# Optimization experiments

Hardware: AMD Instinct MI355X
Metric: run time of the kernel (lower is better)

## Reference

```python
import jax, jax.numpy as jnp
import numpy as np

N_USERS = 100000
N_LOCAS = 50000
N = N_USERS + N_LOCAS
D = 128   # embedding_dynamic_size
K = 128   # kg entity dim
S = 128   # static dim
NK = 50000  # kg rows
E = 2048  # number of events
LN_EPS = 1e-5
NORM_EPS = 1e-12


def setup_inputs() -> dict:
    key = jax.random.key(0)
    ks = jax.random.split(key, 24)
    f = jnp.float32
    rin = D + K + 1
    s_rnn = 1.0 / np.sqrt(D)
    s_pred = 1.0 / np.sqrt(2 * S + 2 * D + K)
    inp = {
        'embedding': jax.random.normal(ks[0], (N, D), f),
        'static': jax.random.normal(ks[1], (N, S), f),
        'kg': jax.random.normal(ks[2], (NK, K), f),
        'W_ih_u': jax.random.normal(ks[3], (D, rin), f) * s_rnn,
        'b_ih_u': jax.random.normal(ks[4], (D,), f) * s_rnn,
        'W_hh_u': jax.random.normal(ks[5], (D, D), f) * s_rnn,
        'b_hh_u': jax.random.normal(ks[6], (D,), f) * s_rnn,
        'W_ih_l': jax.random.normal(ks[7], (D, rin), f) * s_rnn,
        'b_ih_l': jax.random.normal(ks[8], (D,), f) * s_rnn,
        'W_hh_l': jax.random.normal(ks[9], (D, D), f) * s_rnn,
        'b_hh_l': jax.random.normal(ks[10], (D,), f) * s_rnn,
        'w_proj': jax.random.normal(ks[11], (D,), f),   # NormalLinear(1, D) weight, std=1/sqrt(1)=1
        'b_proj': jax.random.normal(ks[12], (D,), f),
        'ln_g': jnp.ones((D + K,), f),
        'ln_b': jnp.zeros((D + K,), f),
        'W_pred': jax.random.normal(ks[13], (S + D, 2 * S + 2 * D + K), f) * s_pred,
        'b_pred': jnp.zeros((S + D,), f),
        'delta_u': jax.random.uniform(ks[14], (E,), f),
        'delta_l': jax.random.uniform(ks[15], (E,), f),
        'idx_user': jax.random.randint(ks[16], (E,), 0, N_USERS, jnp.int32),
        'idx_loca': jax.random.randint(ks[17], (E,), 0, N_LOCAS, jnp.int32),
        'idx_prev': jax.random.randint(ks[18], (E,), 0, N_LOCAS, jnp.int32),
        'idx_know': jax.random.randint(ks[19], (E,), 0, NK, jnp.int32),
        'num_users': N_USERS,
    }
    return inp


def reference(embedding, static, kg, W_ih_u, b_ih_u, W_hh_u, b_hh_u,
              W_ih_l, b_ih_l, W_hh_l, b_hh_l, w_proj, b_proj, ln_g, ln_b,
              W_pred, b_pred, delta_u, delta_l,
              idx_user, idx_loca, idx_prev, idx_know, num_users):
    sg = jax.lax.stop_gradient

    def l2n(x):  # F.normalize along the feature dim (row vector)
        return x / jnp.maximum(jnp.linalg.norm(x), NORM_EPS)

    # event index preprocessing (matches idx_loca + num_users etc.)
    xs = (idx_user, idx_loca + num_users, idx_prev + num_users, idx_know,
          delta_u, delta_l)

    def step(carry, ev):
        emb, loss = carry
        iu, il, ip, ik, du, dl = ev
        u = emb[iu]        # [D]
        l = emb[il]        # [D]
        p = emb[ip]        # [D]
        kgr = kg[ik]       # [K]
        # projection: u * (1 + Linear(1->D)(delta_u))
        proj = u * (1.0 + w_proj * du + b_proj)
        # layer_norm over concat([emb_prev, kg_row]) of size D+K
        x = jnp.concatenate([p, kgr])
        mu = x.mean()
        var = jnp.mean((x - mu) ** 2)
        ln = (x - mu) / jnp.sqrt(var + LN_EPS) * ln_g + ln_b
        meta = jnp.concatenate([proj, ln, static[ip], static[iu]])  # [2S+2D+K]
        pred = W_pred @ meta + b_pred                               # [S+D]
        tgt = jnp.concatenate([l, static[il]])
        loss_pred = jnp.mean((pred - sg(tgt)) ** 2)
        # RNNCell updates (tanh), then L2-normalize
        x_u = jnp.concatenate([l, kgr, du[None]])
        new_u = l2n(jnp.tanh(W_ih_u @ x_u + b_ih_u + W_hh_u @ u + b_hh_u))
        x_l = jnp.concatenate([u, kgr, dl[None]])
        new_l = l2n(jnp.tanh(W_ih_l @ x_l + b_ih_l + W_hh_l @ l + b_hh_l))
        loss = loss + loss_pred \
                    + jnp.mean((new_u - sg(u)) ** 2) \
                    + jnp.mean((new_l - sg(l)) ** 2)
        emb = emb.at[iu].set(new_u).at[il].set(new_l)
        return (emb, loss), None

    (emb, loss), _ = jax.lax.scan(
        step, (embedding, jnp.asarray(0.0, embedding.dtype)), xs)
    return emb, loss
```

## Files before the change

kernel.cpp:

```cpp
#include <hip/hip_runtime.h>

#define DEVINL static __device__ __forceinline__

typedef float f32x4 __attribute__((ext_vector_type(4)));

constexpr int NUSER = 100000;
constexpr int D     = 128;
constexpr int METAN = 640;
constexpr int NT    = 256;
constexpr int CH    = 4;
constexpr int KP4   = 160;
constexpr int KR4   = 96;
constexpr int NCPY  = 2048;
constexpr int STW   = 640;

struct Params {
  const float *emb_in, *stat, *kg;
  const float *Wihu, *bihu, *Whhu, *bhhu;
  const float *Wihl, *bihl, *Whhl, *bhhl;
  const float *wproj, *bproj, *lng, *lnb, *Wpred, *bpred;
  const float *deltau, *deltal;
  const int *idxu, *idxl, *idxp, *idxk;
  float *emb;
  float *loss_slot;
  float *WpredT;
  float *WrnnT;
  float *brnn;
  float *wcol;
  float *loss_ev;
  float *stash;
  int *cnt_u, *cnt_w, *cnt_t;
  int *flag_u, *flag_l;
  int E, N, NLOC, NWORK;
};

DEVINL float loadx(const float* p) {
  return __hip_atomic_load(p, __ATOMIC_RELAXED, __HIP_MEMORY_SCOPE_AGENT);
}
DEVINL void storex(float* p, float v) {
  __hip_atomic_store(p, v, __ATOMIC_RELAXED, __HIP_MEMORY_SCOPE_AGENT);
}
DEVINL int loadcnt(const int* p) {
  return __hip_atomic_load(p, __ATOMIC_RELAXED, __HIP_MEMORY_SCOPE_AGENT);
}
DEVINL void sigadd(int* pp) {
  __hip_atomic_fetch_add(pp, 1, __ATOMIC_RELAXED, __HIP_MEMORY_SCOPE_AGENT);
}
DEVINL float dot4(float4 a, float4 b) { return a.x*b.x + a.y*b.y + a.z*b.z + a.w*b.w; }

DEVINL float4 block_sum4(float4 v, float4* s4) {
  #pragma unroll
  for (int o = 32; o; o >>= 1) {
    v.x += __shfl_xor(v.x, o, 64); v.y += __shfl_xor(v.y, o, 64);
    v.z += __shfl_xor(v.z, o, 64); v.w += __shfl_xor(v.w, o, 64);
  }
  if ((threadIdx.x & 63) == 0) s4[threadIdx.x >> 6] = v;
  __syncthreads();
  float4 r;
  r.x = s4[0].x + s4[1].x + s4[2].x + s4[3].x;
  r.y = s4[0].y + s4[1].y + s4[2].y + s4[3].y;
  r.z = s4[0].z + s4[1].z + s4[2].z + s4[3].z;
  r.w = s4[0].w + s4[1].w + s4[2].w + s4[3].w;
  __syncthreads();
  return r;
}

DEVINL void half_sum4(float4 v, float4* s4, float4* lo, float4* hi) {
  #pragma unroll
  for (int o = 32; o; o >>= 1) {
    v.x += __shfl_xor(v.x, o, 64); v.y += __shfl_xor(v.y, o, 64);
    v.z += __shfl_xor(v.z, o, 64); v.w += __shfl_xor(v.w, o, 64);
  }
  if ((threadIdx.x & 63) == 0) s4[threadIdx.x >> 6] = v;
  __syncthreads();
  lo->x = s4[0].x + s4[1].x; lo->y = s4[0].y + s4[1].y;
  lo->z = s4[0].z + s4[1].z; lo->w = s4[0].w + s4[1].w;
  hi->x = s4[2].x + s4[3].x; hi->y = s4[2].y + s4[3].y;
  hi->z = s4[2].z + s4[3].z; hi->w = s4[2].w + s4[3].w;
  __syncthreads();
}

__global__ void k_init(Params p) {
  int tid = blockIdx.x * NT + threadIdx.x;
  int stride = gridDim.x * NT;
  for (int e = tid; e < p.E; e += stride) {
    p.flag_u[p.idxu[e]] = 1;
    p.flag_l[p.idxl[e]] = 1;
  }
  for (int idx = tid; idx < 256 * KP4; idx += stride) {
    int j = idx / KP4, k4 = idx - j * KP4;
    float4 v = *(const float4*)(p.Wpred + (size_t)j * METAN + k4 * 4);
    ((float4*)p.WpredT)[k4 * 256 + j] = v;
  }
  for (int idx = tid; idx < 256 * KR4; idx += stride) {
    int j = idx / KR4, k4 = idx - j * KR4;
    int i = j & 127;
    const float* Wih = (j < 128) ? p.Wihu : p.Wihl;
    const float* Whh = (j < 128) ? p.Whhu : p.Whhl;
    float4 v; float* vp = (float*)&v;
    #pragma unroll
    for (int e = 0; e < 4; ++e) {
      int k = k4 * 4 + e;
      vp[e] = (k < 256) ? Wih[(size_t)i * 257 + k] : Whh[(size_t)i * 128 + (k - 256)];
    }
    ((float4*)p.WrnnT)[k4 * 256 + j] = v;
  }
  for (int j = tid; j < 256; j += stride) {
    int i = j & 127;
    p.brnn[j] = (j < 128) ? p.bihu[i] + p.bhhu[i] : p.bihl[i] + p.bhhl[i];
    p.wcol[j] = (j < 128) ? p.Wihu[(size_t)i * 257 + 256] : p.Wihl[(size_t)i * 257 + 256];
  }
}

__global__ __launch_bounds__(NT) void k_copy(Params p) {
  size_t gid = (size_t)blockIdx.x * NT + threadIdx.x;
  size_t gs  = (size_t)gridDim.x * NT;
  size_t n4  = (size_t)p.N * 32;
  const f32x4* src = (const f32x4*)p.emb_in;
  f32x4* dst = (f32x4*)p.emb;
  size_t g = gid;
  for (; g + 3 * gs < n4; g += 4 * gs) {
    size_t g0 = g, g1 = g + gs, g2 = g + 2 * gs, g3 = g + 3 * gs;
    int r0 = (int)(g0 >> 5), r1 = (int)(g1 >> 5), r2 = (int)(g2 >> 5), r3 = (int)(g3 >> 5);
    int f0 = (r0 < NUSER) ? p.flag_u[r0] : p.flag_l[r0 - NUSER];
    int f1 = (r1 < NUSER) ? p.flag_u[r1] : p.flag_l[r1 - NUSER];
    int f2 = (r2 < NUSER) ? p.flag_u[r2] : p.flag_l[r2 - NUSER];
    int f3 = (r3 < NUSER) ? p.flag_u[r3] : p.flag_l[r3 - NUSER];
    f32x4 v0 = src[g0], v1 = src[g1], v2 = src[g2], v3 = src[g3];
    if (!f0) dst[g0] = v0;
    if (!f1) dst[g1] = v1;
    if (!f2) dst[g2] = v2;
    if (!f3) dst[g3] = v3;
  }
  for (; g < n4; g += gs) {
    int r = (int)(g >> 5);
    int f = (r < NUSER) ? p.flag_u[r] : p.flag_l[r - NUSER];
    f32x4 v = src[g];
    if (!f) dst[g] = v;
  }
}

__global__ __launch_bounds__(NT, 2) void k_chain(Params p) {
  __shared__ __align__(16) float s_u[CH][D], s_l[CH][D], s_p[CH][D], s_kg[CH][D];
  __shared__ float4 s_r4[4];
  __shared__ unsigned long long s_redu[4][CH];
  __shared__ int s_ev[8][CH];
  __shared__ float s_dd[2][CH];

  const int tid = threadIdx.x, w = tid >> 6, lane = tid & 63;
  const int c = blockIdx.x;
  const int base = c * CH;
  const int nev = min(CH, p.E - base);
  if (nev <= 0) return;

  int iu_[CH], il_[CH], ip_[CH], ik_[CH];
  float du_[CH], dl_[CH];
  #pragma unroll
  for (int e = 0; e < CH; ++e) {
    int t = base + e; bool v = e < nev;
    iu_[e] = v ? p.idxu[t] : -1;
    il_[e] = v ? p.idxl[t] : -1;
    ip_[e] = v ? p.idxp[t] : -1;
    ik_[e] = v ? p.idxk[t] : 0;
    du_[e] = v ? p.deltau[t] : 0.f;
    dl_[e] = v ? p.deltal[t] : 0.f;
  }

  unsigned long long pk[CH] = {0ull,0ull,0ull,0ull};
  for (int s = tid; s < base; s += NT) {
    int ius = p.idxu[s], ils = p.idxl[s], ips = p.idxp[s];
    #pragma unroll
    for (int e = 0; e < CH; ++e) {
      unsigned long long a  = (ius == iu_[e]);
      unsigned long long wl = (ils == il_[e]);
      unsigned long long b  = (unsigned long long)((ils == il_[e]) + (ips == il_[e]));
      unsigned long long cc = (ils == ip_[e]);
      pk[e] += a | (wl << 16) | (b << 32) | (cc << 48);
    }
  }
  #pragma unroll
  for (int o = 32; o; o >>= 1) {
    #pragma unroll
    for (int e = 0; e < CH; ++e) pk[e] += __shfl_xor(pk[e], o, 64);
  }
  if (lane == 0) {
    #pragma unroll
    for (int e = 0; e < CH; ++e) s_redu[w][e] = pk[e];
  }
  __syncthreads();
  #pragma unroll
  for (int e = 0; e < CH; ++e)
    pk[e] = s_redu[0][e] + s_redu[1][e] + s_redu[2][e] + s_redu[3][e];
  __syncthreads();

  int A_[CH], WL_[CH], B_[CH], C_[CH];
  #pragma unroll
  for (int e = 0; e < CH; ++e) {
    int a  = (int)(pk[e] & 0xffff),        wl = (int)((pk[e] >> 16) & 0xffff);
    int b  = (int)((pk[e] >> 32) & 0xffff), cc = (int)((pk[e] >> 48) & 0xffff);
    #pragma unroll
    for (int s2 = 0; s2 < CH; ++s2) if (s2 < e) {
      a  += (iu_[s2] == iu_[e]);
      wl += (il_[s2] == il_[e]);
      b  += (il_[s2] == il_[e]) + (ip_[s2] == il_[e]);
      cc += (il_[s2] == ip_[e]);
    }
    A_[e] = a; WL_[e] = wl; B_[e] = b; C_[e] = cc;
  }
  bool internal = false;
  #pragma unroll
  for (int t2 = 1; t2 < CH; ++t2) if (t2 < nev) {
    #pragma unroll
    for (int s2 = 0; s2 < t2; ++s2)
      internal |= (iu_[s2] == iu_[t2]) | (il_[s2] == il_[t2]) |
                  (il_[s2] == ip_[t2]) | (ip_[s2] == il_[t2]);
  }

  if (tid == 0) {
    #pragma unroll
    for (int e = 0; e < CH; ++e) {
      s_ev[0][e] = iu_[e]; s_ev[1][e] = il_[e]; s_ev[2][e] = ip_[e];
      s_ev[3][e] = A_[e];  s_ev[4][e] = WL_[e]; s_ev[5][e] = B_[e];
      s_ev[6][e] = C_[e];  s_ev[7][e] = ik_[e];
      s_dd[0][e] = du_[e]; s_dd[1][e] = dl_[e];
    }
  }
  __syncthreads();

  auto PRELOAD = [&](int b0, int b1) {
    int e = w;
    if (e >= b0 && e < b1) {
      int iu = s_ev[0][e], ilr = s_ev[1][e] + NUSER, ipr = s_ev[2][e] + NUSER;
      int A = s_ev[3][e], WL = s_ev[4][e], Ck = s_ev[6][e], ik = s_ev[7][e];
      if (lane < 32) {
        int li = lane * 4;
        *(float4*)&s_kg[e][li] = *(const float4*)(p.kg + (size_t)ik * D + li);
      }
      int i0 = lane * 2;
      if (!A)  *(float2*)&s_u[e][i0] = *(const float2*)(p.emb_in + (size_t)iu  * D + i0);
      if (!WL) *(float2*)&s_l[e][i0] = *(const float2*)(p.emb_in + (size_t)ilr * D + i0);
      if (!Ck) *(float2*)&s_p[e][i0] = *(const float2*)(p.emb_in + (size_t)ipr * D + i0);
    }
  };

  auto SPIN = [&](int b0, int b1) {
    if (w == 0) {
      int e = b0 + lane;
      bool act = lane < (b1 - b0);
      int iu = 0, il = 0, ip = 0, A = 0, Bc = 0, Cc = 0;
      if (act) {
        iu = s_ev[0][e]; il = s_ev[1][e]; ip = s_ev[2][e];
        A = s_ev[3][e]; Bc = s_ev[5][e]; Cc = s_ev[6][e];
      }
      int guard = 0;
      while (true) {
        int x = loadcnt(&p.cnt_u[iu]);
        int y = loadcnt(&p.cnt_t[il]);
        int z = loadcnt(&p.cnt_w[ip]);
        bool ok = (!act) | ((x >= A) & (y >= Bc) & (z >= Cc));
        if (__all(ok)) break;
        if (++guard > (1 << 22)) break;
        __builtin_amdgcn_s_sleep(1);
      }
    }
    __syncthreads();
  };

  auto POSTLOAD = [&](int b0, int b1) {
    int e = w;
    if (e >= b0 && e < b1) {
      int iu = s_ev[0][e], ilr = s_ev[1][e] + NUSER, ipr = s_ev[2][e] + NUSER;
      int A = s_ev[3][e], WL = s_ev[4][e], Ck = s_ev[6][e];
      int i0 = lane * 2;
      if (A) {
        s_u[e][i0]   = loadx(p.emb + (size_t)iu * D + i0);
        s_u[e][i0+1] = loadx(p.emb + (size_t)iu * D + i0 + 1);
      }
      if (WL) {
        s_l[e][i0]   = loadx(p.emb + (size_t)ilr * D + i0);
        s_l[e][i0+1] = loadx(p.emb + (size_t)ilr * D + i0 + 1);
      }
      if (Ck) {
        s_p[e][i0]   = loadx(p.emb + (size_t)ipr * D + i0);
        s_p[e][i0+1] = loadx(p.emb + (size_t)ipr * D + i0 + 1);
      }
    }
  };

  auto RNNPROC = [&](int b0, int b1) {
    __syncthreads();
    const bool uc = (tid < 128);
    const float4* xo0 = (const float4*)(uc ? s_l[0] : s_u[0]);
    const float4* xo1 = (const float4*)(uc ? s_l[1] : s_u[1]);
    const float4* xo2 = (const float4*)(uc ? s_l[2] : s_u[2]);
    const float4* xo3 = (const float4*)(uc ? s_l[3] : s_u[3]);
    const float4* xk0 = (const float4*)s_kg[0];
    const float4* xk1 = (const float4*)s_kg[1];
    const float4* xk2 = (const float4*)s_kg[2];
    const float4* xk3 = (const float4*)s_kg[3];
    const float4* xs0 = (const float4*)(uc ? s_u[0] : s_l[0]);
    const float4* xs1 = (const float4*)(uc ? s_u[1] : s_l[1]);
    const float4* xs2 = (const float4*)(uc ? s_u[2] : s_l[2]);
    const float4* xs3 = (const float4*)(uc ? s_u[3] : s_l[3]);
    float ra0 = 0.f, ra1 = 0.f, ra2 = 0.f, ra3 = 0.f;
    const float4* wr = (const float4*)p.WrnnT + tid;
    #pragma unroll 8
    for (int k4 = 0; k4 < 32; ++k4) {
      float4 wv = wr[k4 * 256];
      ra0 += dot4(wv, xo0[k4]); ra1 += dot4(wv, xo1[k4]);
      ra2 += dot4(wv, xo2[k4]); ra3 += dot4(wv, xo3[k4]);
    }
    #pragma unroll 8
    for (int k4 = 32; k4 < 64; ++k4) {
      float4 wv = wr[k4 * 256];
      ra0 += dot4(wv, xk0[k4-32]); ra1 += dot4(wv, xk1[k4-32]);
      ra2 += dot4(wv, xk2[k4-32]); ra3 += dot4(wv, xk3[k4-32]);
    }
    #pragma unroll 8
    for (int k4 = 64; k4 < 96; ++k4) {
      float4 wv = wr[k4 * 256];
      ra0 += dot4(wv, xs0[k4-64]); ra1 += dot4(wv, xs1[k4-64]);
      ra2 += dot4(wv, xs2[k4-64]); ra3 += dot4(wv, xs3[k4-64]);
    }
    float brn = p.brnn[tid], wcv = p.wcol[tid];
    float d0 = uc ? s_dd[0][0] : s_dd[1][0];
    float d1 = uc ? s_dd[0][1] : s_dd[1][1];
    float d2 = uc ? s_dd[0][2] : s_dd[1][2];
    float d3 = uc ? s_dd[0][3] : s_dd[1][3];
    float h0 = tanhf(ra0 + brn + wcv * d0), h1 = tanhf(ra1 + brn + wcv * d1);
    float h2v = tanhf(ra2 + brn + wcv * d2), h3 = tanhf(ra3 + brn + wcv * d3);

    float4 SU, SL;
    half_sum4(make_float4(h0*h0, h1*h1, h2v*h2v, h3*h3), s_r4, &SU, &SL);
    float s0 = uc ? SU.x : SL.x, s1 = uc ? SU.y : SL.y;
    float s2 = uc ? SU.z : SL.z, s3 = uc ? SU.w : SL.w;
    float n0 = h0 / fmaxf(sqrtf(s0), 1e-12f), n1 = h1 / fmaxf(sqrtf(s1), 1e-12f);
    float n2 = h2v / fmaxf(sqrtf(s2), 1e-12f), n3 = h3 / fmaxf(sqrtf(s3), 1e-12f);

    float nv[CH] = {n0, n1, n2, n3};
    #pragma unroll
    for (int e = 0; e < CH; ++e) if (e >= b0 && e < b1) {
      if (tid < 128) storex(p.emb + (size_t)s_ev[0][e] * D + tid, nv[e]);
      else           storex(p.emb + ((size_t)s_ev[1][e] + NUSER) * D + (tid - 128), nv[e]);
    }
    __syncthreads();

    if (tid >= b0 && tid < b1) {
      __builtin_amdgcn_fence(__ATOMIC_RELEASE, "agent");
      sigadd(&p.cnt_u[s_ev[0][tid]]);
      sigadd(&p.cnt_t[s_ev[1][tid]]);
      sigadd(&p.cnt_w[s_ev[1][tid]]);
      sigadd(&p.cnt_t[s_ev[2][tid]]);
    }

    #pragma unroll
    for (int e = 0; e < CH; ++e) if (e >= b0 && e < b1) {
      float* st = p.stash + (size_t)(base + e) * STW;
      if (tid < 128) {
        st[tid]       = s_u[e][tid];
        st[256 + tid] = s_p[e][tid];
        st[384 + tid] = nv[e];
      } else {
        int i = tid - 128;
        st[128 + i] = s_l[e][i];
        st[512 + i] = nv[e];
      }
    }
  };

  if (!internal) {
    PRELOAD(0, nev);
    SPIN(0, nev);
    POSTLOAD(0, nev);
    RNNPROC(0, nev);
  } else {
    for (int e = 0; e < nev; ++e) {
      PRELOAD(e, e + 1);
      SPIN(e, e + 1);
      POSTLOAD(e, e + 1);
      RNNPROC(e, e + 1);
    }
  }
}

__global__ __launch_bounds__(NT, 2) void k_loss(Params p) {
  __shared__ __align__(16) float s_meta[CH][METAN];
  __shared__ __align__(16) float s_u[CH][D], s_l[CH][D], s_p[CH][D], s_kg[CH][D], s_sil[CH][D];
  __shared__ float4 s_r4[4];

  const int tid = threadIdx.x, w = tid >> 6, lane = tid & 63;
  const int c = blockIdx.x;
  const int base = c * CH;
  const int nev = min(CH, p.E - base);
  if (nev <= 0) return;

  if (w < nev) {
    int e = w;
    int t = base + e;
    int iu = p.idxu[t], ilr = p.idxl[t] + NUSER, ipr = p.idxp[t] + NUSER, ik = p.idxk[t];
    const float* st = p.stash + (size_t)t * STW;
    int i0 = lane * 2;
    *(float2*)&s_u[e][i0] = *(const float2*)(st + i0);
    *(float2*)&s_l[e][i0] = *(const float2*)(st + 128 + i0);
    *(float2*)&s_p[e][i0] = *(const float2*)(st + 256 + i0);
    int h2 = lane >> 5, li = (lane & 31) * 4;
    if (h2 == 0) {
      *(float4*)&s_kg[e][li]         = *(const float4*)(p.kg   + (size_t)ik  * D + li);
      *(float4*)&s_meta[e][512 + li] = *(const float4*)(p.stat + (size_t)iu  * D + li);
    } else {
      *(float4*)&s_meta[e][384 + li] = *(const float4*)(p.stat + (size_t)ipr * D + li);
      *(float4*)&s_sil[e][li]        = *(const float4*)(p.stat + (size_t)ilr * D + li);
    }
  }
  __syncthreads();

  if (w < nev) {
    int e = w;
    float du = p.deltau[base + e];
    float4 xv = (lane < 32) ? *(const float4*)&s_p[e][lane * 4]
                            : *(const float4*)&s_kg[e][(lane - 32) * 4];
    float sm = xv.x + xv.y + xv.z + xv.w;
    #pragma unroll
    for (int o = 32; o; o >>= 1) sm += __shfl_xor(sm, o, 64);
    float mu = sm * (1.f / 256.f);
    float4 d = make_float4(xv.x - mu, xv.y - mu, xv.z - mu, xv.w - mu);
    float vs = d.x*d.x + d.y*d.y + d.z*d.z + d.w*d.w;
    #pragma unroll
    for (int o = 32; o; o >>= 1) vs += __shfl_xor(vs, o, 64);
    float rstd = rsqrtf(vs * (1.f / 256.f) + 1e-5f);
    int idx2 = lane * 4;
    float4 g  = *(const float4*)&p.lng[idx2];
    float4 bb = *(const float4*)&p.lnb[idx2];
    *(float4*)&s_meta[e][128 + idx2] = make_float4(
      d.x*rstd*g.x + bb.x, d.y*rstd*g.y + bb.y,
      d.z*rstd*g.z + bb.z, d.w*rstd*g.w + bb.w);
    int i0 = lane * 2;
    #pragma unroll
    for (int j = 0; j < 2; ++j) {
      int i = i0 + j;
      s_meta[e][i] = s_u[e][i] * (1.f + p.wproj[i] * du + p.bproj[i]);
    }
  }
  __syncthreads();

  const bool uc = (tid < 128);
  const float4* m40 = (const float4*)&s_meta[0][0];
  const float4* m41 = (const float4*)&s_meta[1][0];
  const float4* m42 = (const float4*)&s_meta[2][0];
  const float4* m43 = (const float4*)&s_meta[3][0];
  float pa0 = 0.f, pa1 = 0.f, pa2 = 0.f, pa3 = 0.f;
  const float4* wp = (const float4*)p.WpredT + tid;
  #pragma unroll 8
  for (int k4 = 0; k4 < KP4; ++k4) {
    float4 wv = wp[k4 * 256];
    pa0 += dot4(wv, m40[k4]); pa1 += dot4(wv, m41[k4]);
    pa2 += dot4(wv, m42[k4]); pa3 += dot4(wv, m43[k4]);
  }
  float bp = p.bpred[tid];
  float4 ep2;
  {
    float tg0 = uc ? s_l[0][tid] : s_sil[0][tid - 128];
    float tg1 = uc ? s_l[1][tid] : s_sil[1][tid - 128];
    float tg2 = uc ? s_l[2][tid] : s_sil[2][tid - 128];
    float tg3 = uc ? s_l[3][tid] : s_sil[3][tid - 128];
    float e0 = pa0 + bp - tg0, e1 = pa1 + bp - tg1;
    float e2 = pa2 + bp - tg2, e3 = pa3 + bp - tg3;
    ep2 = make_float4(e0*e0, e1*e1, e2*e2, e3*e3);
  }
  float4 LP = block_sum4(ep2, s_r4);

  const float* st0 = p.stash + (size_t)(base + 0) * STW;
  const float* st1 = p.stash + (size_t)(base + 1) * STW;
  const float* st2 = p.stash + (size_t)(base + 2) * STW;
  const float* st3 = p.stash + (size_t)(base + 3) * STW;
  int noff = uc ? (384 + tid) : (512 + tid - 128);
  float n0 = st0[noff], n1 = (nev > 1) ? st1[noff] : 0.f;
  float n2 = (nev > 2) ? st2[noff] : 0.f, n3 = (nev > 3) ? st3[noff] : 0.f;
  float o0 = uc ? s_u[0][tid] : s_l[0][tid - 128];
  float o1 = uc ? s_u[1][tid] : s_l[1][tid - 128];
  float o2 = uc ? s_u[2][tid] : s_l[2][tid - 128];
  float o3 = uc ? s_u[3][tid] : s_l[3][tid - 128];
  float q0 = n0 - o0, q1 = n1 - o1, q2 = n2 - o2, q3 = n3 - o3;
  float4 LE = block_sum4(make_float4(q0*q0, q1*q1, q2*q2, q3*q3), s_r4);

  if (tid < nev) {
    float lp = (tid == 0) ? LP.x : (tid == 1) ? LP.y : (tid == 2) ? LP.z : LP.w;
    float le = (tid == 0) ? LE.x : (tid == 1) ? LE.y : (tid == 2) ? LE.z : LE.w;
    p.loss_ev[base + tid] = lp * (1.f / 256.f) + le * (1.f / 128.f);
  }
}

__global__ void k_fin(Params p) {
  __shared__ float4 s_r4[4];
  float v = 0.f;
  for (int i = threadIdx.x; i < p.E; i += NT) v += p.loss_ev[i];
  float4 r = block_sum4(make_float4(v, 0.f, 0.f, 0.f), s_r4);
  if (threadIdx.x == 0) p.loss_slot[0] = r.x;
}

extern "C" void kernel_launch(void* const* d_in, const int* in_sizes, int n_in,
                              void* d_out, int out_size, void* d_ws, size_t ws_size,
                              hipStream_t stream) {
  Params p;
  p.emb_in = (const float*)d_in[0];
  p.stat   = (const float*)d_in[1];
  p.kg     = (const float*)d_in[2];
  p.Wihu = (const float*)d_in[3];   p.bihu = (const float*)d_in[4];
  p.Whhu = (const float*)d_in[5];   p.bhhu = (const float*)d_in[6];
  p.Wihl = (const float*)d_in[7];   p.bihl = (const float*)d_in[8];
  p.Whhl = (const float*)d_in[9];   p.bhhl = (const float*)d_in[10];
  p.wproj = (const float*)d_in[11]; p.bproj = (const float*)d_in[12];
  p.lng  = (const float*)d_in[13];  p.lnb  = (const float*)d_in[14];
  p.Wpred = (const float*)d_in[15]; p.bpred = (const float*)d_in[16];
  p.deltau = (const float*)d_in[17];
  p.deltal = (const float*)d_in[18];
  p.idxu = (const int*)d_in[19];
  p.idxl = (const int*)d_in[20];
  p.idxp = (const int*)d_in[21];
  p.idxk = (const int*)d_in[22];

  p.E    = in_sizes[17];
  p.N    = in_sizes[0] / D;
  p.NLOC = p.N - NUSER;
  p.NWORK = (p.E + CH - 1) / CH;

  p.emb       = (float*)d_out;
  p.loss_slot = (float*)d_out + (size_t)p.N * D;

  char* ws = (char*)d_ws;
  size_t off = 0;
  auto take = [&](size_t bytes) {
    void* r = ws + off;
    off += (bytes + 255) & ~(size_t)255;
    return r;
  };
  p.WpredT  = (float*)take((size_t)KP4 * 256 * 16);
  p.WrnnT   = (float*)take((size_t)KR4 * 256 * 16);
  p.brnn    = (float*)take(256 * 4);
  p.wcol    = (float*)take(256 * 4);
  p.loss_ev = (float*)take((size_t)p.E * 4);
  p.stash   = (float*)take((size_t)p.E * STW * 4);
  size_t z0 = off;
  p.cnt_u   = (int*)take((size_t)NUSER * 4);
  p.cnt_w   = (int*)take((size_t)p.NLOC * 4);
  p.cnt_t   = (int*)take((size_t)p.NLOC * 4);
  p.flag_u  = (int*)take((size_t)NUSER * 4);
  p.flag_l  = (int*)take((size_t)p.NLOC * 4);
  size_t zbytes = off - z0;

  hipMemsetAsync(ws + z0, 0, zbytes, stream);
  hipLaunchKernelGGL(k_init,  dim3(512),     dim3(NT), 0, stream, p);
  hipLaunchKernelGGL(k_chain, dim3(p.NWORK), dim3(NT), 0, stream, p);
  hipLaunchKernelGGL(k_copy,  dim3(NCPY),    dim3(NT), 0, stream, p);
  hipLaunchKernelGGL(k_loss,  dim3(p.NWORK), dim3(NT), 0, stream, p);
  hipLaunchKernelGGL(k_fin,   dim3(1),       dim3(NT), 0, stream, p);
}
```

Before: 178.2 us.

## Split chain into scan, dependency-free easy pass, and spinning hard pass

Measured after the change: 150.3 us. -15.6%, faster.

```diff
diff --git a/kernel.cpp b/kernel.cpp
--- a/kernel.cpp
+++ b/kernel.cpp
@@ -13,6 +13,7 @@
 constexpr int KR4   = 96;
 constexpr int NCPY  = 2048;
 constexpr int STW   = 640;
+constexpr int CIW   = 20;
 
 struct Params {
   const float *emb_in, *stat, *kg;
@@ -29,6 +30,7 @@
   float *wcol;
   float *loss_ev;
   float *stash;
+  int *cinfo;
   int *cnt_u, *cnt_w, *cnt_t;
   int *flag_u, *flag_l;
   int E, N, NLOC, NWORK;
@@ -112,60 +114,21 @@
   }
 }
 
-__global__ __launch_bounds__(NT) void k_copy(Params p) {
-  size_t gid = (size_t)blockIdx.x * NT + threadIdx.x;
-  size_t gs  = (size_t)gridDim.x * NT;
-  size_t n4  = (size_t)p.N * 32;
-  const f32x4* src = (const f32x4*)p.emb_in;
-  f32x4* dst = (f32x4*)p.emb;
-  size_t g = gid;
-  for (; g + 3 * gs < n4; g += 4 * gs) {
-    size_t g0 = g, g1 = g + gs, g2 = g + 2 * gs, g3 = g + 3 * gs;
-    int r0 = (int)(g0 >> 5), r1 = (int)(g1 >> 5), r2 = (int)(g2 >> 5), r3 = (int)(g3 >> 5);
-    int f0 = (r0 < NUSER) ? p.flag_u[r0] : p.flag_l[r0 - NUSER];
-    int f1 = (r1 < NUSER) ? p.flag_u[r1] : p.flag_l[r1 - NUSER];
-    int f2 = (r2 < NUSER) ? p.flag_u[r2] : p.flag_l[r2 - NUSER];
-    int f3 = (r3 < NUSER) ? p.flag_u[r3] : p.flag_l[r3 - NUSER];
-    f32x4 v0 = src[g0], v1 = src[g1], v2 = src[g2], v3 = src[g3];
-    if (!f0) dst[g0] = v0;
-    if (!f1) dst[g1] = v1;
-    if (!f2) dst[g2] = v2;
-    if (!f3) dst[g3] = v3;
-  }
-  for (; g < n4; g += gs) {
-    int r = (int)(g >> 5);
-    int f = (r < NUSER) ? p.flag_u[r] : p.flag_l[r - NUSER];
-    f32x4 v = src[g];
-    if (!f) dst[g] = v;
-  }
-}
-
-__global__ __launch_bounds__(NT, 2) void k_chain(Params p) {
-  __shared__ __align__(16) float s_u[CH][D], s_l[CH][D], s_p[CH][D], s_kg[CH][D];
-  __shared__ float4 s_r4[4];
+__global__ __launch_bounds__(NT) void k_scan(Params p) {
   __shared__ unsigned long long s_redu[4][CH];
-  __shared__ int s_ev[8][CH];
-  __shared__ float s_dd[2][CH];
-
   const int tid = threadIdx.x, w = tid >> 6, lane = tid & 63;
-  const int c = blockIdx.x;
-  const int base = c * CH;
+  const int c = blockIdx.x, base = c * CH;
   const int nev = min(CH, p.E - base);
   if (nev <= 0) return;
 
-  int iu_[CH], il_[CH], ip_[CH], ik_[CH];
-  float du_[CH], dl_[CH];
+  int iu_[CH], il_[CH], ip_[CH];
   #pragma unroll
   for (int e = 0; e < CH; ++e) {
     int t = base + e; bool v = e < nev;
     iu_[e] = v ? p.idxu[t] : -1;
     il_[e] = v ? p.idxl[t] : -1;
     ip_[e] = v ? p.idxp[t] : -1;
-    ik_[e] = v ? p.idxk[t] : 0;
-    du_[e] = v ? p.deltau[t] : 0.f;
-    dl_[e] = v ? p.deltal[t] : 0.f;
-  }
-
+  }
   unsigned long long pk[CH] = {0ull,0ull,0ull,0ull};
   for (int s = tid; s < base; s += NT) {
     int ius = p.idxu[s], ils = p.idxl[s], ips = p.idxp[s];
@@ -191,38 +154,178 @@
   #pragma unroll
   for (int e = 0; e < CH; ++e)
     pk[e] = s_redu[0][e] + s_redu[1][e] + s_redu[2][e] + s_redu[3][e];
-  __syncthreads();
-
-  int A_[CH], WL_[CH], B_[CH], C_[CH];
+
+  if (tid == 0) {
+    int* ci = p.cinfo + (size_t)c * CIW;
+    bool internal = false;
+    #pragma unroll
+    for (int t2 = 1; t2 < CH; ++t2) if (t2 < nev) {
+      #pragma unroll
+      for (int s2 = 0; s2 < t2; ++s2)
+        internal |= (iu_[s2] == iu_[t2]) | (il_[s2] == il_[t2]) |
+                    (il_[s2] == ip_[t2]) | (ip_[s2] == il_[t2]);
+    }
+    bool clean = !internal;
+    #pragma unroll
+    for (int e = 0; e < CH; ++e) {
+      int a  = (int)(pk[e] & 0xffff),        wl = (int)((pk[e] >> 16) & 0xffff);
+      int b  = (int)((pk[e] >> 32) & 0xffff), cc = (int)((pk[e] >> 48) & 0xffff);
+      #pragma unroll
+      for (int s2 = 0; s2 < CH; ++s2) if (s2 < e) {
+        a  += (iu_[s2] == iu_[e]);
+        wl += (il_[s2] == il_[e]);
+        b  += (il_[s2] == il_[e]) + (ip_[s2] == il_[e]);
+        cc += (il_[s2] == ip_[e]);
+      }
+      ci[e] = a; ci[4 + e] = wl; ci[8 + e] = b; ci[12 + e] = cc;
+      if (e < nev) clean = clean && (a == 0) && (b == 0) && (cc == 0);
+    }
+    ci[16] = internal ? 1 : 0;
+    ci[17] = clean ? 1 : 0;
+  }
+}
+
+__global__ __launch_bounds__(NT, 2) void k_easy(Params p) {
+  __shared__ __align__(16) float s_u[CH][D], s_l[CH][D], s_p[CH][D], s_kg[CH][D];
+  __shared__ float4 s_r4[4];
+  __shared__ int s_ev[3][CH];
+  __shared__ float s_dd[2][CH];
+
+  const int tid = threadIdx.x, w = tid >> 6, lane = tid & 63;
+  const int c = blockIdx.x, base = c * CH;
+  const int nev = min(CH, p.E - base);
+  if (nev <= 0) return;
+  if (!p.cinfo[(size_t)c * CIW + 17]) return;
+
+  if (tid == 0) {
+    #pragma unroll
+    for (int e = 0; e < CH; ++e) {
+      int t = base + e; bool v = e < nev;
+      s_ev[0][e] = v ? p.idxu[t] : 0;
+      s_ev[1][e] = v ? p.idxl[t] : 0;
+      s_ev[2][e] = v ? p.idxk[t] : 0;
+      s_dd[0][e] = v ? p.deltau[t] : 0.f;
+      s_dd[1][e] = v ? p.deltal[t] : 0.f;
+    }
+  }
+  __syncthreads();
+
+  if (w < nev) {
+    int e = w;
+    int t = base + e;
+    int iu = s_ev[0][e], ilr = s_ev[1][e] + NUSER, ipr = p.idxp[t] + NUSER, ik = s_ev[2][e];
+    if (lane < 32) {
+      int li = lane * 4;
+      *(float4*)&s_kg[e][li] = *(const float4*)(p.kg + (size_t)ik * D + li);
+    }
+    int i0 = lane * 2;
+    *(float2*)&s_u[e][i0] = *(const float2*)(p.emb_in + (size_t)iu  * D + i0);
+    *(float2*)&s_l[e][i0] = *(const float2*)(p.emb_in + (size_t)ilr * D + i0);
+    *(float2*)&s_p[e][i0] = *(const float2*)(p.emb_in + (size_t)ipr * D + i0);
+  }
+  __syncthreads();
+
+  const bool uc = (tid < 128);
+  const float4* xo0 = (const float4*)(uc ? s_l[0] : s_u[0]);
+  const float4* xo1 = (const float4*)(uc ? s_l[1] : s_u[1]);
+  const float4* xo2 = (const float4*)(uc ? s_l[2] : s_u[2]);
+  const float4* xo3 = (const float4*)(uc ? s_l[3] : s_u[3]);
+  const float4* xk0 = (const float4*)s_kg[0];
+  const float4* xk1 = (const float4*)s_kg[1];
+  const float4* xk2 = (const float4*)s_kg[2];
+  const float4* xk3 = (const float4*)s_kg[3];
+  const float4* xs0 = (const float4*)(uc ? s_u[0] : s_l[0]);
+  const float4* xs1 = (const float4*)(uc ? s_u[1] : s_l[1]);
+  const float4* xs2 = (const float4*)(uc ? s_u[2] : s_l[2]);
+  const float4* xs3 = (const float4*)(uc ? s_u[3] : s_l[3]);
+  float ra0 = 0.f, ra1 = 0.f, ra2 = 0.f, ra3 = 0.f;
+  const float4* wr = (const float4*)p.WrnnT + tid;
+  #pragma unroll 8
+  for (int k4 = 0; k4 < 32; ++k4) {
+    float4 wv = wr[k4 * 256];
+    ra0 += dot4(wv, xo0[k4]); ra1 += dot4(wv, xo1[k4]);
+    ra2 += dot4(wv, xo2[k4]); ra3 += dot4(wv, xo3[k4]);
+  }
+  #pragma unroll 8
+  for (int k4 = 32; k4 < 64; ++k4) {
+    float4 wv = wr[k4 * 256];
+    ra0 += dot4(wv, xk0[k4-32]); ra1 += dot4(wv, xk1[k4-32]);
+    ra2 += dot4(wv, xk2[k4-32]); ra3 += dot4(wv, xk3[k4-32]);
+  }
+  #pragma unroll 8
+  for (int k4 = 64; k4 < 96; ++k4) {
+    float4 wv = wr[k4 * 256];
+    ra0 += dot4(wv, xs0[k4-64]); ra1 += dot4(wv, xs1[k4-64]);
+    ra2 += dot4(wv, xs2[k4-64]); ra3 += dot4(wv, xs3[k4-64]);
+  }
+  float brn = p.brnn[tid], wcv = p.wcol[tid];
+  float d0 = uc ? s_dd[0][0] : s_dd[1][0];
+  float d1 = uc ? s_dd[0][1] : s_dd[1][1];
+  float d2 = uc ? s_dd[0][2] : s_dd[1][2];
+  float d3 = uc ? s_dd[0][3] : s_dd[1][3];
+  float h0 = tanhf(ra0 + brn + wcv * d0), h1 = tanhf(ra1 + brn + wcv * d1);
+  float h2v = tanhf(ra2 + brn + wcv * d2), h3 = tanhf(ra3 + brn + wcv * d3);
+
+  float4 SU, SL;
+  half_sum4(make_float4(h0*h0, h1*h1, h2v*h2v, h3*h3), s_r4, &SU, &SL);
+  float s0 = uc ? SU.x : SL.x, s1 = uc ? SU.y : SL.y;
+  float s2 = uc ? SU.z : SL.z, s3 = uc ? SU.w : SL.w;
+  float n0 = h0 / fmaxf(sqrtf(s0), 1e-12f), n1 = h1 / fmaxf(sqrtf(s1), 1e-12f);
+  float n2 = h2v / fmaxf(sqrtf(s2), 1e-12f), n3 = h3 / fmaxf(sqrtf(s3), 1e-12f);
+
+  float nv[CH] = {n0, n1, n2, n3};
   #pragma unroll
-  for (int e = 0; e < CH; ++e) {
-    int a  = (int)(pk[e] & 0xffff),        wl = (int)((pk[e] >> 16) & 0xffff);
-    int b  = (int)((pk[e] >> 32) & 0xffff), cc = (int)((pk[e] >> 48) & 0xffff);
-    #pragma unroll
-    for (int s2 = 0; s2 < CH; ++s2) if (s2 < e) {
-      a  += (iu_[s2] == iu_[e]);
-      wl += (il_[s2] == il_[e]);
-      b  += (il_[s2] == il_[e]) + (ip_[s2] == il_[e]);
-      cc += (il_[s2] == ip_[e]);
-    }
-    A_[e] = a; WL_[e] = wl; B_[e] = b; C_[e] = cc;
-  }
-  bool internal = false;
-  #pragma unroll
-  for (int t2 = 1; t2 < CH; ++t2) if (t2 < nev) {
-    #pragma unroll
-    for (int s2 = 0; s2 < t2; ++s2)
-      internal |= (iu_[s2] == iu_[t2]) | (il_[s2] == il_[t2]) |
-                  (il_[s2] == ip_[t2]) | (ip_[s2] == il_[t2]);
-  }
+  for (int e = 0; e < CH; ++e) if (e < nev) {
+    if (tid < 128) p.emb[(size_t)s_ev[0][e] * D + tid] = nv[e];
+    else           p.emb[((size_t)s_ev[1][e] + NUSER) * D + (tid - 128)] = nv[e];
+    float* st = p.stash + (size_t)(base + e) * STW;
+    if (tid < 128) {
+      st[tid]       = s_u[e][tid];
+      st[256 + tid] = s_p[e][tid];
+      st[384 + tid] = nv[e];
+    } else {
+      int i = tid - 128;
+      st[128 + i] = s_l[e][i];
+      st[512 + i] = nv[e];
+    }
+  }
+
+  if (tid < nev) {
+    sigadd(&p.cnt_u[s_ev[0][tid]]);
+    sigadd(&p.cnt_t[s_ev[1][tid]]);
+    sigadd(&p.cnt_w[s_ev[1][tid]]);
+    sigadd(&p.cnt_t[p.idxp[base + tid]]);
+  }
+}
+
+__global__ __launch_bounds__(NT, 2) void k_hard(Params p) {
+  __shared__ __align__(16) float s_u[CH][D], s_l[CH][D], s_p[CH][D], s_kg[CH][D];
+  __shared__ float4 s_r4[4];
+  __shared__ int s_ev[8][CH];
+  __shared__ float s_dd[2][CH];
+
+  const int tid = threadIdx.x, w = tid >> 6, lane = tid & 63;
+  const int c = blockIdx.x, base = c * CH;
+  const int nev = min(CH, p.E - base);
+  if (nev <= 0) return;
+  const int* ci = p.cinfo + (size_t)c * CIW;
+  if (ci[17]) return;
+  const bool internal = ci[16];
 
   if (tid == 0) {
     #pragma unroll
     for (int e = 0; e < CH; ++e) {
-      s_ev[0][e] = iu_[e]; s_ev[1][e] = il_[e]; s_ev[2][e] = ip_[e];
-      s_ev[3][e] = A_[e];  s_ev[4][e] = WL_[e]; s_ev[5][e] = B_[e];
-      s_ev[6][e] = C_[e];  s_ev[7][e] = ik_[e];
-      s_dd[0][e] = du_[e]; s_dd[1][e] = dl_[e];
+      int t = base + e; bool v = e < nev;
+      s_ev[0][e] = v ? p.idxu[t] : 0;
+      s_ev[1][e] = v ? p.idxl[t] : 0;
+      s_ev[2][e] = v ? p.idxp[t] : 0;
+      s_ev[3][e] = ci[e];
+      s_ev[4][e] = ci[4 + e];
+      s_ev[5][e] = ci[8 + e];
+      s_ev[6][e] = ci[12 + e];
+      s_ev[7][e] = v ? p.idxk[t] : 0;
+      s_dd[0][e] = v ? p.deltau[t] : 0.f;
+      s_dd[1][e] = v ? p.deltal[t] : 0.f;
     }
   }
   __syncthreads();
@@ -383,6 +486,34 @@
   }
 }
 
+__global__ __launch_bounds__(NT) void k_copy(Params p) {
+  size_t gid = (size_t)blockIdx.x * NT + threadIdx.x;
+  size_t gs  = (size_t)gridDim.x * NT;
+  size_t n4  = (size_t)p.N * 32;
+  const f32x4* src = (const f32x4*)p.emb_in;
+  f32x4* dst = (f32x4*)p.emb;
+  size_t g = gid;
+  for (; g + 3 * gs < n4; g += 4 * gs) {
+    size_t g0 = g, g1 = g + gs, g2 = g + 2 * gs, g3 = g + 3 * gs;
+    int r0 = (int)(g0 >> 5), r1 = (int)(g1 >> 5), r2 = (int)(g2 >> 5), r3 = (int)(g3 >> 5);
+    int f0 = (r0 < NUSER) ? p.flag_u[r0] : p.flag_l[r0 - NUSER];
+    int f1 = (r1 < NUSER) ? p.flag_u[r1] : p.flag_l[r1 - NUSER];
+    int f2 = (r2 < NUSER) ? p.flag_u[r2] : p.flag_l[r2 - NUSER];
+    int f3 = (r3 < NUSER) ? p.flag_u[r3] : p.flag_l[r3 - NUSER];
+    f32x4 v0 = src[g0], v1 = src[g1], v2 = src[g2], v3 = src[g3];
+    if (!f0) dst[g0] = v0;
+    if (!f1) dst[g1] = v1;
+    if (!f2) dst[g2] = v2;
+    if (!f3) dst[g3] = v3;
+  }
+  for (; g < n4; g += gs) {
+    int r = (int)(g >> 5);
+    int f = (r < NUSER) ? p.flag_u[r] : p.flag_l[r - NUSER];
+    f32x4 v = src[g];
+    if (!f) dst[g] = v;
+  }
+}
+
 __global__ __launch_bounds__(NT, 2) void k_loss(Params p) {
   __shared__ __align__(16) float s_meta[CH][METAN];
   __shared__ __align__(16) float s_u[CH][D], s_l[CH][D], s_p[CH][D], s_kg[CH][D], s_sil[CH][D];
@@ -540,6 +671,7 @@
   p.wcol    = (float*)take(256 * 4);
   p.loss_ev = (float*)take((size_t)p.E * 4);
   p.stash   = (float*)take((size_t)p.E * STW * 4);
+  p.cinfo   = (int*)take((size_t)p.NWORK * CIW * 4);
   size_t z0 = off;
   p.cnt_u   = (int*)take((size_t)NUSER * 4);
   p.cnt_w   = (int*)take((size_t)p.NLOC * 4);
@@ -550,8 +682,10 @@
 
   hipMemsetAsync(ws + z0, 0, zbytes, stream);
   hipLaunchKernelGGL(k_init,  dim3(512),     dim3(NT), 0, stream, p);
-  hipLaunchKernelGGL(k_chain, dim3(p.NWORK), dim3(NT), 0, stream, p);
+  hipLaunchKernelGGL(k_scan,  dim3(p.NWORK), dim3(NT), 0, stream, p);
+  hipLaunchKernelGGL(k_easy,  dim3(p.NWORK), dim3(NT), 0, stream, p);
+  hipLaunchKernelGGL(k_hard,  dim3(p.NWORK), dim3(NT), 0, stream, p);
+  hipLaunchKernelGGL(k_loss,  dim3(p.NWORK), dim3(NT), 0, stream, p);
   hipLaunchKernelGGL(k_copy,  dim3(NCPY),    dim3(NT), 0, stream, p);
-  hipLaunchKernelGGL(k_loss,  dim3(p.NWORK), dim3(NT), 0, stream, p);
   hipLaunchKernelGGL(k_fin,   dim3(1),       dim3(NT), 0, stream, p);
 }
```
